# Performance work log

Measured on AMD Instinct MI355X. Metric: run time of the kernel, lower is better.

Reference implementation:

```python
import jax, jax.numpy as jnp
import numpy as np

N_NODES = 50000
N_EDGES = 800000
D = 128


def setup_inputs() -> dict:
    key = jax.random.key(0)
    ks = jax.random.split(key, 8)
    s = 1.0 / np.sqrt(D)
    return {
        "x": jax.random.normal(ks[0], (N_NODES, D), dtype=jnp.float32),
        "edge_index": jax.random.randint(ks[1], (2, N_EDGES), 0, N_NODES, dtype=jnp.int32),
        "W0l": jax.random.normal(ks[2], (D, D), dtype=jnp.float32) * s,
        "b0l": jnp.zeros((D,), dtype=jnp.float32),
        "W0r": jax.random.normal(ks[3], (D, D), dtype=jnp.float32) * s,
        "W1l": jax.random.normal(ks[4], (D, D), dtype=jnp.float32) * s,
        "b1l": jnp.zeros((D,), dtype=jnp.float32),
        "W1r": jax.random.normal(ks[5], (D, D), dtype=jnp.float32) * s,
    }


def reference(x, edge_index, W0l, b0l, W0r, W1l, b1l, W1r):
    # Encoder(conv='sage', num_layers=2), eval mode (dropout = identity).
    src = edge_index[0]  # x_j gathered from source nodes
    dst = edge_index[1]  # aggregated at target nodes
    # in-degree for mean aggregation; isolated nodes get 0 aggregate (PyG mean)
    deg = jax.ops.segment_sum(jnp.ones_like(dst, dtype=x.dtype), dst, num_segments=N_NODES)
    inv_deg = jnp.where(deg > 0, 1.0 / jnp.maximum(deg, 1.0), 0.0)[:, None]

    def sage(h, Wl, bl, Wr):
        m = h @ Wl + bl                                        # lin_l
        agg = jax.ops.segment_sum(m[src], dst, num_segments=N_NODES) * inv_deg  # mean aggr
        return agg + h @ Wr                                    # + lin_r skip

    h = jax.nn.relu(sage(x, W0l, b0l, W0r))   # layer 0 + relu
    return sage(h, W1l, b1l, W1r)             # final layer
```

## Files before the change

### kernel.cpp

```cpp
#include <hip/hip_runtime.h>

#define N_NODES 50000
#define N_EDGES 800000
#define D 128
#define NBLK ((N_NODES + 255) / 256)
#define EPB 4096
#define CAP 8192

typedef __bf16 bf16x8 __attribute__((ext_vector_type(8)));
typedef short s16x8 __attribute__((ext_vector_type(8)));
typedef float f32x4 __attribute__((ext_vector_type(4)));
typedef unsigned short u16;
typedef unsigned int u32;
typedef u32 u32x2 __attribute__((ext_vector_type(2)));
typedef u32 u32x4 __attribute__((ext_vector_type(4)));

__device__ inline u16 f32_to_bf16(float f) {
    u32 u = __builtin_bit_cast(u32, f);
    u += 0x7fffu + ((u >> 16) & 1u);
    return (u16)(u >> 16);
}
__device__ inline float bf16_lo(u32 v) { return __builtin_bit_cast(float, v << 16); }
__device__ inline float bf16_hi(u32 v) { return __builtin_bit_cast(float, v & 0xffff0000u); }

__device__ inline f32x4 mfma16(s16x8 a, s16x8 b, f32x4 c) {
    return __builtin_amdgcn_mfma_f32_16x16x32_bf16(
        __builtin_bit_cast(bf16x8, a), __builtin_bit_cast(bf16x8, b), c, 0, 0, 0);
}

#define CAST_BLOCKS ((N_NODES * 16) / 256)
#define STAGE_BLOCKS ((N_EDGES + EPB - 1) / EPB)

__global__ __launch_bounds__(256) void prep_stage(
    const float* __restrict__ x, u16* __restrict__ xb,
    const float* __restrict__ W0l, const float* __restrict__ W0r,
    const float* __restrict__ W1l, const float* __restrict__ W1r,
    u16* __restrict__ Wp,
    const int* __restrict__ src, const int* __restrict__ dst,
    int* __restrict__ ccount, u32* __restrict__ staged) {
    __shared__ int hist[NBLK];
    __shared__ int base[NBLK];
    int t = threadIdx.x, b = blockIdx.x;
    if (b < CAST_BLOCKS) {
        int gid = b * 256 + t;
        const float* p = x + (size_t)gid * 8;
        f32x4 a = *(const f32x4*)p;
        f32x4 c = *(const f32x4*)(p + 4);
        u16 o[8];
#pragma unroll
        for (int j = 0; j < 4; j++) { o[j] = f32_to_bf16(a[j]); o[4 + j] = f32_to_bf16(c[j]); }
        *(s16x8*)(xb + (size_t)gid * 8) = *(const s16x8*)o;
    } else if (b < CAST_BLOCKS + 32) {
        int gid = (b - CAST_BLOCKS) * 256 + t;
        int wsel = gid >> 11;
        int rem  = gid & 2047;
        int ct   = rem >> 8;
        int ks   = (rem >> 6) & 3;
        int lane = rem & 63;
        const float* W = (wsel == 0) ? W0l : (wsel == 1) ? W0r : (wsel == 2) ? W1l : W1r;
        int n  = ct * 16 + (lane & 15);
        int k0 = ks * 32 + (lane >> 4) * 8;
        u16 o[8];
#pragma unroll
        for (int j = 0; j < 8; j++) o[j] = f32_to_bf16(W[(k0 + j) * D + n]);
        u16* dp = Wp + wsel * 16384 + (size_t)((ct * 4 + ks) * 64 + lane) * 8;
        *(s16x8*)dp = *(const s16x8*)o;
    } else {
        int sb = b - CAST_BLOCKS - 32;
        int bb = sb * EPB;
        if (t < NBLK) hist[t] = 0;
        __syncthreads();
        u32 pk[16]; int cb[16];
#pragma unroll
        for (int i = 0; i < 16; i++) {
            int e = bb + i * 256 + t;
            if (e < N_EDGES) {
                int sv = src[e], dv = dst[e];
                pk[i] = (u32)sv | ((u32)(dv & 255) << 16);
                cb[i] = dv >> 8;
                atomicAdd(&hist[cb[i]], 1);
            } else cb[i] = -1;
        }
        __syncthreads();
        if (t < NBLK) {
            int c = hist[t];
            if (c > 0) {
                int old = atomicAdd(&ccount[t], c);
                if (old > CAP - c) old = CAP - c;
                base[t] = t * CAP + old;
            }
            hist[t] = 0;
        }
        __syncthreads();
#pragma unroll
        for (int i = 0; i < 16; i++) {
            if (cb[i] >= 0) {
                int slot = atomicAdd(&hist[cb[i]], 1);
                staged[base[cb[i]] + slot] = pk[i];
            }
        }
    }
}

__global__ __launch_bounds__(256) void fine_kernel(const int* __restrict__ ccount,
                                                   const u32* __restrict__ staged,
                                                   u16* __restrict__ eidx,
                                                   int* __restrict__ rowptr,
                                                   float* __restrict__ inv) {
    __shared__ u32 sdata[CAP];
    __shared__ int hist[256];
    __shared__ int cursor[256];
    __shared__ int sc[256];
    __shared__ int wsum[4];
    int t = threadIdx.x, cb = blockIdx.x;
    int lane = t & 63, wave = t >> 6;

    int cc = (t < NBLK) ? ccount[t] : 0;
    int cv = cc > CAP ? CAP : cc;
    int s = cv;
#pragma unroll
    for (int off = 1; off < 64; off <<= 1) {
        int u = __shfl_up(s, off, 64);
        if (lane >= off) s += u;
    }
    if (lane == 63) wsum[wave] = s;
    hist[t] = 0;
    __syncthreads();
    int wadd = 0;
#pragma unroll
    for (int w = 0; w < 4; w++) if (w < wave) wadd += wsum[w];
    sc[t] = s - cv + wadd;
    __syncthreads();
    int gbase = sc[cb];
    int c = ccount[cb];
    if (c > CAP) c = CAP;

    for (int i = t; i < c; i += 256) {
        u32 v = staged[cb * CAP + i];
        sdata[i] = v;
        atomicAdd(&hist[(v >> 16) & 255], 1);
    }
    __syncthreads();
    int d = hist[t];
    s = d;
#pragma unroll
    for (int off = 1; off < 64; off <<= 1) {
        int u = __shfl_up(s, off, 64);
        if (lane >= off) s += u;
    }
    if (lane == 63) wsum[wave] = s;
    __syncthreads();
    wadd = 0;
#pragma unroll
    for (int w = 0; w < 4; w++) if (w < wave) wadd += wsum[w];
    int excl = gbase + s - d + wadd;
    int node = cb * 256 + t;
    if (node < N_NODES) {
        rowptr[node] = excl;
        inv[node] = d > 0 ? 1.0f / (float)d : 0.0f;
    }
    cursor[t] = excl;
    if (cb == 0 && t == 0) rowptr[N_NODES] = N_EDGES;
    __syncthreads();
    for (int i = t; i < c; i += 256) {
        u32 v = sdata[i];
        int pos = atomicAdd(&cursor[(v >> 16) & 255], 1);
        eidx[pos] = (u16)(v & 0xffffu);
    }
}

__global__ __launch_bounds__(256) void agg_mean(const u16* __restrict__ h,
                                                const int* __restrict__ rowptr,
                                                const u16* __restrict__ eidx,
                                                const float* __restrict__ inv,
                                                u16* __restrict__ mean) {
    int wave = threadIdx.x >> 6, lane = threadIdx.x & 63;
    int node = blockIdx.x * 4 + wave;
    if (node >= N_NODES) return;
    int quad = lane >> 4;
    int ql = lane & 15;
    int start = rowptr[node], end = rowptr[node + 1];

    float a0=0.f,a1=0.f,a2=0.f,a3=0.f,a4=0.f,a5=0.f,a6=0.f,a7=0.f;
    int base = start;
    for (; base + 16 <= end; base += 16) {
        int i0 = base + quad;
        int s0 = eidx[i0], s1 = eidx[i0 + 4], s2 = eidx[i0 + 8], s3 = eidx[i0 + 12];
        u32x4 v0 = *(const u32x4*)(h + (size_t)s0 * D + ql * 8);
        u32x4 v1 = *(const u32x4*)(h + (size_t)s1 * D + ql * 8);
        u32x4 v2 = *(const u32x4*)(h + (size_t)s2 * D + ql * 8);
        u32x4 v3 = *(const u32x4*)(h + (size_t)s3 * D + ql * 8);
        a0 += bf16_lo(v0.x) + bf16_lo(v1.x) + bf16_lo(v2.x) + bf16_lo(v3.x);
        a1 += bf16_hi(v0.x) + bf16_hi(v1.x) + bf16_hi(v2.x) + bf16_hi(v3.x);
        a2 += bf16_lo(v0.y) + bf16_lo(v1.y) + bf16_lo(v2.y) + bf16_lo(v3.y);
        a3 += bf16_hi(v0.y) + bf16_hi(v1.y) + bf16_hi(v2.y) + bf16_hi(v3.y);
        a4 += bf16_lo(v0.z) + bf16_lo(v1.z) + bf16_lo(v2.z) + bf16_lo(v3.z);
        a5 += bf16_hi(v0.z) + bf16_hi(v1.z) + bf16_hi(v2.z) + bf16_hi(v3.z);
        a6 += bf16_lo(v0.w) + bf16_lo(v1.w) + bf16_lo(v2.w) + bf16_lo(v3.w);
        a7 += bf16_hi(v0.w) + bf16_hi(v1.w) + bf16_hi(v2.w) + bf16_hi(v3.w);
    }
    for (; base < end; base += 4) {
        int i = base + quad;
        if (i < end) {
            u32x4 v = *(const u32x4*)(h + (size_t)eidx[i] * D + ql * 8);
            a0 += bf16_lo(v.x); a1 += bf16_hi(v.x);
            a2 += bf16_lo(v.y); a3 += bf16_hi(v.y);
            a4 += bf16_lo(v.z); a5 += bf16_hi(v.z);
            a6 += bf16_lo(v.w); a7 += bf16_hi(v.w);
        }
    }
    a0 += __shfl_xor(a0, 16); a0 += __shfl_xor(a0, 32);
    a1 += __shfl_xor(a1, 16); a1 += __shfl_xor(a1, 32);
    a2 += __shfl_xor(a2, 16); a2 += __shfl_xor(a2, 32);
    a3 += __shfl_xor(a3, 16); a3 += __shfl_xor(a3, 32);
    a4 += __shfl_xor(a4, 16); a4 += __shfl_xor(a4, 32);
    a5 += __shfl_xor(a5, 16); a5 += __shfl_xor(a5, 32);
    a6 += __shfl_xor(a6, 16); a6 += __shfl_xor(a6, 32);
    a7 += __shfl_xor(a7, 16); a7 += __shfl_xor(a7, 32);

    if (quad == 0) {
        float iv = inv[node];
        u32x4 o;
        o.x = (u32)f32_to_bf16(a0 * iv) | ((u32)f32_to_bf16(a1 * iv) << 16);
        o.y = (u32)f32_to_bf16(a2 * iv) | ((u32)f32_to_bf16(a3 * iv) << 16);
        o.z = (u32)f32_to_bf16(a4 * iv) | ((u32)f32_to_bf16(a5 * iv) << 16);
        o.w = (u32)f32_to_bf16(a6 * iv) | ((u32)f32_to_bf16(a7 * iv) << 16);
        *(u32x4*)(mean + (size_t)node * D + ql * 8) = o;
    }
}

template <int RELU, int OUTF32>
__global__ __launch_bounds__(256) void gemm_fused(
    const u16* __restrict__ A1, const u16* __restrict__ A2,
    const u16* __restrict__ WpR, const u16* __restrict__ WpL,
    const float* __restrict__ bias, const float* __restrict__ inv,
    u16* __restrict__ outb, float* __restrict__ outf, int M) {
    int wave = threadIdx.x >> 6, lane = threadIdx.x & 63;
    int rowbase = blockIdx.x * 64;
    int lrow = lane & 15, quad = lane >> 4;

    s16x8 bR[2][4], bL[2][4];
#pragma unroll
    for (int ct = 0; ct < 2; ct++) {
        int ctg = wave * 2 + ct;
#pragma unroll
        for (int ks = 0; ks < 4; ks++) {
            size_t off = (size_t)((ctg * 4 + ks) * 64 + lane) * 8;
            bR[ct][ks] = *(const s16x8*)(WpR + off);
            bL[ct][ks] = *(const s16x8*)(WpL + off);
        }
    }

    f32x4 acc[4][2];
#pragma unroll
    for (int rt = 0; rt < 4; rt++)
#pragma unroll
        for (int ct = 0; ct < 2; ct++) acc[rt][ct] = (f32x4){0.f, 0.f, 0.f, 0.f};

#pragma unroll
    for (int ks = 0; ks < 4; ks++) {
        s16x8 a1[4], a2[4];
#pragma unroll
        for (int rt = 0; rt < 4; rt++) {
            int row = rowbase + rt * 16 + lrow;
            row = row < M ? row : M - 1;
            a1[rt] = *(const s16x8*)(A1 + (size_t)row * D + ks * 32 + quad * 8);
            a2[rt] = *(const s16x8*)(A2 + (size_t)row * D + ks * 32 + quad * 8);
        }
#pragma unroll
        for (int rt = 0; rt < 4; rt++)
#pragma unroll
            for (int ct = 0; ct < 2; ct++) {
                acc[rt][ct] = mfma16(a1[rt], bR[ct][ks], acc[rt][ct]);
                acc[rt][ct] = mfma16(a2[rt], bL[ct][ks], acc[rt][ct]);
            }
    }

    float bv[2];
#pragma unroll
    for (int ct = 0; ct < 2; ct++) bv[ct] = bias[wave * 32 + ct * 16 + lrow];

#pragma unroll
    for (int rt = 0; rt < 4; rt++) {
#pragma unroll
        for (int i = 0; i < 4; i++) {
            int row = rowbase + rt * 16 + quad * 4 + i;
            if (row >= M) continue;
            float mask = inv[row] > 0.f ? 1.f : 0.f;
#pragma unroll
            for (int ct = 0; ct < 2; ct++) {
                int col = wave * 32 + ct * 16 + lrow;
                float v = acc[rt][ct][i] + mask * bv[ct];
                if (RELU) v = v > 0.f ? v : 0.f;
                if (OUTF32) outf[(size_t)row * D + col] = v;
                else        outb[(size_t)row * D + col] = f32_to_bf16(v);
            }
        }
    }
}

extern "C" void kernel_launch(void* const* d_in, const int* in_sizes, int n_in,
                              void* d_out, int out_size, void* d_ws, size_t ws_size,
                              hipStream_t stream) {
    const float* x    = (const float*)d_in[0];
    const int*   edge = (const int*)d_in[1];
    const int*   src  = edge;
    const int*   dstn = edge + N_EDGES;
    const float* W0l  = (const float*)d_in[2];
    const float* b0l  = (const float*)d_in[3];
    const float* W0r  = (const float*)d_in[4];
    const float* W1l  = (const float*)d_in[5];
    const float* b1l  = (const float*)d_in[6];
    const float* W1r  = (const float*)d_in[7];
    float* out = (float*)d_out;

    char* p = (char*)d_ws;
    auto alloc = [&](size_t nb) { char* r = p; p += (nb + 255) & ~(size_t)255; return r; };
    int*   ccount = (int*)alloc((size_t)NBLK * 4);
    int*   rowptr = (int*)alloc((size_t)(N_NODES + 1) * 4);
    float* inv    = (float*)alloc((size_t)N_NODES * 4);
    u32*   staged = (u32*)alloc((size_t)NBLK * CAP * 4);
    u16*   eidx   = (u16*)alloc((size_t)N_EDGES * 2);
    u16*   xb     = (u16*)alloc((size_t)N_NODES * D * 2);
    u16*   hb     = (u16*)alloc((size_t)N_NODES * D * 2);
    u16*   meanb  = (u16*)alloc((size_t)N_NODES * D * 2);
    u16*   Wp     = (u16*)alloc((size_t)4 * 16384 * 2);

    hipMemsetAsync(ccount, 0, (size_t)NBLK * 4, stream);

    prep_stage<<<CAST_BLOCKS + 32 + STAGE_BLOCKS, 256, 0, stream>>>(
        x, xb, W0l, W0r, W1l, W1r, Wp, src, dstn, ccount, staged);
    fine_kernel<<<NBLK, 256, 0, stream>>>(ccount, staged, eidx, rowptr, inv);

    int mblocks = (N_NODES + 63) / 64;
    int ablocks = (N_NODES + 3) / 4;
    const u16* WpL0 = Wp;
    const u16* WpR0 = Wp + 16384;
    const u16* WpL1 = Wp + 2 * 16384;
    const u16* WpR1 = Wp + 3 * 16384;
    agg_mean<<<ablocks, 256, 0, stream>>>(xb, rowptr, eidx, inv, meanb);
    gemm_fused<1, 0><<<mblocks, 256, 0, stream>>>(xb, meanb, WpR0, WpL0, b0l, inv, hb, nullptr, N_NODES);
    agg_mean<<<ablocks, 256, 0, stream>>>(hb, rowptr, eidx, inv, meanb);
    gemm_fused<0, 1><<<mblocks, 256, 0, stream>>>(hb, meanb, WpR1, WpL1, b1l, inv, nullptr, out, N_NODES);
}
```

Measured before the change: 222.5 us.

## Fuse mean aggregation into GEMM kernel via LDS-staged tile

Merges the aggregation and GEMM kernels per layer into one kernel. Each block first gathers and averages neighbours for 16 nodes into an XOR-swizzled LDS tile, then runs MFMA over the self features and the LDS mean. This removes the round trip of the mean buffer through global memory and two kernel launches per layer. In exchange, each block serialises four nodes per wave before the GEMM, and every block of 16 rows reloads the full weight fragments, which raises weight traffic and may reduce latency hiding.

```diff
diff --git a/kernel.cpp b/kernel.cpp
--- a/kernel.cpp
+++ b/kernel.cpp
@@ -12,7 +12,6 @@
 typedef float f32x4 __attribute__((ext_vector_type(4)));
 typedef unsigned short u16;
 typedef unsigned int u32;
-typedef u32 u32x2 __attribute__((ext_vector_type(2)));
 typedef u32 u32x4 __attribute__((ext_vector_type(4)));
 
 __device__ inline u16 f32_to_bf16(float f) {
@@ -169,75 +168,69 @@
     }
 }
 
-__global__ __launch_bounds__(256) void agg_mean(const u16* __restrict__ h,
-                                                const int* __restrict__ rowptr,
-                                                const u16* __restrict__ eidx,
-                                                const float* __restrict__ inv,
-                                                u16* __restrict__ mean) {
-    int wave = threadIdx.x >> 6, lane = threadIdx.x & 63;
-    int node = blockIdx.x * 4 + wave;
-    if (node >= N_NODES) return;
-    int quad = lane >> 4;
-    int ql = lane & 15;
-    int start = rowptr[node], end = rowptr[node + 1];
-
-    float a0=0.f,a1=0.f,a2=0.f,a3=0.f,a4=0.f,a5=0.f,a6=0.f,a7=0.f;
-    int base = start;
-    for (; base + 16 <= end; base += 16) {
-        int i0 = base + quad;
-        int s0 = eidx[i0], s1 = eidx[i0 + 4], s2 = eidx[i0 + 8], s3 = eidx[i0 + 12];
-        u32x4 v0 = *(const u32x4*)(h + (size_t)s0 * D + ql * 8);
-        u32x4 v1 = *(const u32x4*)(h + (size_t)s1 * D + ql * 8);
-        u32x4 v2 = *(const u32x4*)(h + (size_t)s2 * D + ql * 8);
-        u32x4 v3 = *(const u32x4*)(h + (size_t)s3 * D + ql * 8);
-        a0 += bf16_lo(v0.x) + bf16_lo(v1.x) + bf16_lo(v2.x) + bf16_lo(v3.x);
-        a1 += bf16_hi(v0.x) + bf16_hi(v1.x) + bf16_hi(v2.x) + bf16_hi(v3.x);
-        a2 += bf16_lo(v0.y) + bf16_lo(v1.y) + bf16_lo(v2.y) + bf16_lo(v3.y);
-        a3 += bf16_hi(v0.y) + bf16_hi(v1.y) + bf16_hi(v2.y) + bf16_hi(v3.y);
-        a4 += bf16_lo(v0.z) + bf16_lo(v1.z) + bf16_lo(v2.z) + bf16_lo(v3.z);
-        a5 += bf16_hi(v0.z) + bf16_hi(v1.z) + bf16_hi(v2.z) + bf16_hi(v3.z);
-        a6 += bf16_lo(v0.w) + bf16_lo(v1.w) + bf16_lo(v2.w) + bf16_lo(v3.w);
-        a7 += bf16_hi(v0.w) + bf16_hi(v1.w) + bf16_hi(v2.w) + bf16_hi(v3.w);
-    }
-    for (; base < end; base += 4) {
-        int i = base + quad;
-        if (i < end) {
-            u32x4 v = *(const u32x4*)(h + (size_t)eidx[i] * D + ql * 8);
-            a0 += bf16_lo(v.x); a1 += bf16_hi(v.x);
-            a2 += bf16_lo(v.y); a3 += bf16_hi(v.y);
-            a4 += bf16_lo(v.z); a5 += bf16_hi(v.z);
-            a6 += bf16_lo(v.w); a7 += bf16_hi(v.w);
-        }
-    }
-    a0 += __shfl_xor(a0, 16); a0 += __shfl_xor(a0, 32);
-    a1 += __shfl_xor(a1, 16); a1 += __shfl_xor(a1, 32);
-    a2 += __shfl_xor(a2, 16); a2 += __shfl_xor(a2, 32);
-    a3 += __shfl_xor(a3, 16); a3 += __shfl_xor(a3, 32);
-    a4 += __shfl_xor(a4, 16); a4 += __shfl_xor(a4, 32);
-    a5 += __shfl_xor(a5, 16); a5 += __shfl_xor(a5, 32);
-    a6 += __shfl_xor(a6, 16); a6 += __shfl_xor(a6, 32);
-    a7 += __shfl_xor(a7, 16); a7 += __shfl_xor(a7, 32);
-
-    if (quad == 0) {
-        float iv = inv[node];
-        u32x4 o;
-        o.x = (u32)f32_to_bf16(a0 * iv) | ((u32)f32_to_bf16(a1 * iv) << 16);
-        o.y = (u32)f32_to_bf16(a2 * iv) | ((u32)f32_to_bf16(a3 * iv) << 16);
-        o.z = (u32)f32_to_bf16(a4 * iv) | ((u32)f32_to_bf16(a5 * iv) << 16);
-        o.w = (u32)f32_to_bf16(a6 * iv) | ((u32)f32_to_bf16(a7 * iv) << 16);
-        *(u32x4*)(mean + (size_t)node * D + ql * 8) = o;
-    }
-}
-
 template <int RELU, int OUTF32>
-__global__ __launch_bounds__(256) void gemm_fused(
-    const u16* __restrict__ A1, const u16* __restrict__ A2,
+__global__ __launch_bounds__(256) void fused_layer(
+    const u16* __restrict__ A,
     const u16* __restrict__ WpR, const u16* __restrict__ WpL,
     const float* __restrict__ bias, const float* __restrict__ inv,
-    u16* __restrict__ outb, float* __restrict__ outf, int M) {
+    const int* __restrict__ rowptr, const u16* __restrict__ eidx,
+    u16* __restrict__ outb, float* __restrict__ outf) {
+    __shared__ char mlds[16 * 256];
     int wave = threadIdx.x >> 6, lane = threadIdx.x & 63;
-    int rowbase = blockIdx.x * 64;
-    int lrow = lane & 15, quad = lane >> 4;
+    int rowbase = blockIdx.x * 16;
+    int quad = lane >> 4, ql = lane & 15;
+
+#pragma unroll 1
+    for (int i = 0; i < 4; i++) {
+        int node = rowbase + wave * 4 + i;
+        int start = rowptr[node], end = rowptr[node + 1];
+        float a0=0.f,a1=0.f,a2=0.f,a3=0.f,a4=0.f,a5=0.f,a6=0.f,a7=0.f;
+        int base = start;
+        for (; base + 16 <= end; base += 16) {
+            int i0 = base + quad;
+            int s0 = eidx[i0], s1 = eidx[i0 + 4], s2 = eidx[i0 + 8], s3 = eidx[i0 + 12];
+            u32x4 v0 = *(const u32x4*)(A + (size_t)s0 * D + ql * 8);
+            u32x4 v1 = *(const u32x4*)(A + (size_t)s1 * D + ql * 8);
+            u32x4 v2 = *(const u32x4*)(A + (size_t)s2 * D + ql * 8);
+            u32x4 v3 = *(const u32x4*)(A + (size_t)s3 * D + ql * 8);
+            a0 += bf16_lo(v0.x) + bf16_lo(v1.x) + bf16_lo(v2.x) + bf16_lo(v3.x);
+            a1 += bf16_hi(v0.x) + bf16_hi(v1.x) + bf16_hi(v2.x) + bf16_hi(v3.x);
+            a2 += bf16_lo(v0.y) + bf16_lo(v1.y) + bf16_lo(v2.y) + bf16_lo(v3.y);
+            a3 += bf16_hi(v0.y) + bf16_hi(v1.y) + bf16_hi(v2.y) + bf16_hi(v3.y);
+            a4 += bf16_lo(v0.z) + bf16_lo(v1.z) + bf16_lo(v2.z) + bf16_lo(v3.z);
+            a5 += bf16_hi(v0.z) + bf16_hi(v1.z) + bf16_hi(v2.z) + bf16_hi(v3.z);
+            a6 += bf16_lo(v0.w) + bf16_lo(v1.w) + bf16_lo(v2.w) + bf16_lo(v3.w);
+            a7 += bf16_hi(v0.w) + bf16_hi(v1.w) + bf16_hi(v2.w) + bf16_hi(v3.w);
+        }
+        for (; base < end; base += 4) {
+            int ii = base + quad;
+            if (ii < end) {
+                u32x4 v = *(const u32x4*)(A + (size_t)eidx[ii] * D + ql * 8);
+                a0 += bf16_lo(v.x); a1 += bf16_hi(v.x);
+                a2 += bf16_lo(v.y); a3 += bf16_hi(v.y);
+                a4 += bf16_lo(v.z); a5 += bf16_hi(v.z);
+                a6 += bf16_lo(v.w); a7 += bf16_hi(v.w);
+            }
+        }
+        a0 += __shfl_xor(a0, 16); a0 += __shfl_xor(a0, 32);
+        a1 += __shfl_xor(a1, 16); a1 += __shfl_xor(a1, 32);
+        a2 += __shfl_xor(a2, 16); a2 += __shfl_xor(a2, 32);
+        a3 += __shfl_xor(a3, 16); a3 += __shfl_xor(a3, 32);
+        a4 += __shfl_xor(a4, 16); a4 += __shfl_xor(a4, 32);
+        a5 += __shfl_xor(a5, 16); a5 += __shfl_xor(a5, 32);
+        a6 += __shfl_xor(a6, 16); a6 += __shfl_xor(a6, 32);
+        a7 += __shfl_xor(a7, 16); a7 += __shfl_xor(a7, 32);
+        if (quad == 0) {
+            float iv = inv[node];
+            u32x4 o;
+            o.x = (u32)f32_to_bf16(a0 * iv) | ((u32)f32_to_bf16(a1 * iv) << 16);
+            o.y = (u32)f32_to_bf16(a2 * iv) | ((u32)f32_to_bf16(a3 * iv) << 16);
+            o.z = (u32)f32_to_bf16(a4 * iv) | ((u32)f32_to_bf16(a5 * iv) << 16);
+            o.w = (u32)f32_to_bf16(a6 * iv) | ((u32)f32_to_bf16(a7 * iv) << 16);
+            int lr = wave * 4 + i;
+            *(u32x4*)(mlds + lr * 256 + ((ql ^ lr) & 15) * 16) = o;
+        }
+    }
 
     s16x8 bR[2][4], bL[2][4];
 #pragma unroll
@@ -250,51 +243,37 @@
             bL[ct][ks] = *(const s16x8*)(WpL + off);
         }
     }
-
-    f32x4 acc[4][2];
-#pragma unroll
-    for (int rt = 0; rt < 4; rt++)
-#pragma unroll
-        for (int ct = 0; ct < 2; ct++) acc[rt][ct] = (f32x4){0.f, 0.f, 0.f, 0.f};
-
+    __syncthreads();
+
+    f32x4 acc[2];
+    acc[0] = (f32x4){0.f, 0.f, 0.f, 0.f};
+    acc[1] = (f32x4){0.f, 0.f, 0.f, 0.f};
 #pragma unroll
     for (int ks = 0; ks < 4; ks++) {
-        s16x8 a1[4], a2[4];
-#pragma unroll
-        for (int rt = 0; rt < 4; rt++) {
-            int row = rowbase + rt * 16 + lrow;
-            row = row < M ? row : M - 1;
-            a1[rt] = *(const s16x8*)(A1 + (size_t)row * D + ks * 32 + quad * 8);
-            a2[rt] = *(const s16x8*)(A2 + (size_t)row * D + ks * 32 + quad * 8);
-        }
-#pragma unroll
-        for (int rt = 0; rt < 4; rt++)
-#pragma unroll
-            for (int ct = 0; ct < 2; ct++) {
-                acc[rt][ct] = mfma16(a1[rt], bR[ct][ks], acc[rt][ct]);
-                acc[rt][ct] = mfma16(a2[rt], bL[ct][ks], acc[rt][ct]);
-            }
+        s16x8 a1 = *(const s16x8*)(A + (size_t)(rowbase + ql) * D + ks * 32 + quad * 8);
+        s16x8 a2 = *(const s16x8*)(mlds + ql * 256 + (((ks * 4 + quad) ^ ql) & 15) * 16);
+#pragma unroll
+        for (int ct = 0; ct < 2; ct++) {
+            acc[ct] = mfma16(a1, bR[ct][ks], acc[ct]);
+            acc[ct] = mfma16(a2, bL[ct][ks], acc[ct]);
+        }
     }
 
     float bv[2];
 #pragma unroll
-    for (int ct = 0; ct < 2; ct++) bv[ct] = bias[wave * 32 + ct * 16 + lrow];
-
-#pragma unroll
-    for (int rt = 0; rt < 4; rt++) {
-#pragma unroll
-        for (int i = 0; i < 4; i++) {
-            int row = rowbase + rt * 16 + quad * 4 + i;
-            if (row >= M) continue;
-            float mask = inv[row] > 0.f ? 1.f : 0.f;
-#pragma unroll
-            for (int ct = 0; ct < 2; ct++) {
-                int col = wave * 32 + ct * 16 + lrow;
-                float v = acc[rt][ct][i] + mask * bv[ct];
-                if (RELU) v = v > 0.f ? v : 0.f;
-                if (OUTF32) outf[(size_t)row * D + col] = v;
-                else        outb[(size_t)row * D + col] = f32_to_bf16(v);
-            }
+    for (int ct = 0; ct < 2; ct++) bv[ct] = bias[wave * 32 + ct * 16 + ql];
+
+#pragma unroll
+    for (int i = 0; i < 4; i++) {
+        int row = rowbase + quad * 4 + i;
+        float mask = inv[row] > 0.f ? 1.f : 0.f;
+#pragma unroll
+        for (int ct = 0; ct < 2; ct++) {
+            int col = wave * 32 + ct * 16 + ql;
+            float v = acc[ct][i] + mask * bv[ct];
+            if (RELU) v = v > 0.f ? v : 0.f;
+            if (OUTF32) outf[(size_t)row * D + col] = v;
+            else        outb[(size_t)row * D + col] = f32_to_bf16(v);
         }
     }
 }
@@ -323,7 +302,6 @@
     u16*   eidx   = (u16*)alloc((size_t)N_EDGES * 2);
     u16*   xb     = (u16*)alloc((size_t)N_NODES * D * 2);
     u16*   hb     = (u16*)alloc((size_t)N_NODES * D * 2);
-    u16*   meanb  = (u16*)alloc((size_t)N_NODES * D * 2);
     u16*   Wp     = (u16*)alloc((size_t)4 * 16384 * 2);
 
     hipMemsetAsync(ccount, 0, (size_t)NBLK * 4, stream);
@@ -332,14 +310,11 @@
         x, xb, W0l, W0r, W1l, W1r, Wp, src, dstn, ccount, staged);
     fine_kernel<<<NBLK, 256, 0, stream>>>(ccount, staged, eidx, rowptr, inv);
 
-    int mblocks = (N_NODES + 63) / 64;
-    int ablocks = (N_NODES + 3) / 4;
+    int fblocks = N_NODES / 16;
     const u16* WpL0 = Wp;
     const u16* WpR0 = Wp + 16384;
     const u16* WpL1 = Wp + 2 * 16384;
     const u16* WpR1 = Wp + 3 * 16384;
-    agg_mean<<<ablocks, 256, 0, stream>>>(xb, rowptr, eidx, inv, meanb);
-    gemm_fused<1, 0><<<mblocks, 256, 0, stream>>>(xb, meanb, WpR0, WpL0, b0l, inv, hb, nullptr, N_NODES);
-    agg_mean<<<ablocks, 256, 0, stream>>>(hb, rowptr, eidx, inv, meanb);
-    gemm_fused<0, 1><<<mblocks, 256, 0, stream>>>(hb, meanb, WpR1, WpL1, b1l, inv, nullptr, out, N_NODES);
-}
+    fused_layer<1, 0><<<fblocks, 256, 0, stream>>>(xb, WpR0, WpL0, b0l, inv, rowptr, eidx, hb, nullptr);
+    fused_layer<0, 1><<<fblocks, 256, 0, stream>>>(hb, WpR1, WpL1, b1l, inv, rowptr, eidx, nullptr, out);
+}
```

Result: no change. 218.9 us (-1.6%).
